# Performance work log

Hardware: AMD Instinct MI355X
Metric: run time of the kernel (lower is better)

Reference implementation:

```python
import jax, jax.numpy as jnp
import numpy as np

EMBED_DIM = 768
NUM_HEADS = 12
HEAD_DIM = EMBED_DIM // NUM_HEADS
B, S = 2, 2048


def setup_inputs() -> dict:
    key = jax.random.key(0)
    ks = jax.random.split(key, 6)
    glorot = jnp.sqrt(6.0 / (EMBED_DIM + EMBED_DIM)).astype(jnp.float32)
    x = jax.random.normal(ks[0], (B, S, EMBED_DIM), dtype=jnp.float32)
    mask = jnp.zeros((1, 1, S, S), dtype=jnp.float32)  # additive mask, 0 = no masking
    Wq = jax.random.uniform(ks[1], (EMBED_DIM, EMBED_DIM), jnp.float32, -glorot, glorot)
    Wk = jax.random.uniform(ks[2], (EMBED_DIM, EMBED_DIM), jnp.float32, -glorot, glorot)
    Wv = jax.random.uniform(ks[3], (EMBED_DIM, EMBED_DIM), jnp.float32, -glorot, glorot)
    Wo = jax.random.uniform(ks[4], (EMBED_DIM, EMBED_DIM), jnp.float32, -glorot, glorot)
    bo = jnp.zeros((EMBED_DIM,), dtype=jnp.float32)
    return {"x": x, "mask": mask, "Wq": Wq, "Wk": Wk, "Wv": Wv, "Wo": Wo, "bo": bo}


def reference(x, mask, Wq, Wk, Wv, Wo, bo):
    b, s, _ = x.shape
    # Q/K/V projections (no bias), split into heads: [b, h, s, d]
    def split_heads(t):
        return t.reshape(b, s, NUM_HEADS, HEAD_DIM).transpose(0, 2, 1, 3)
    q = split_heads(x @ Wq)
    k = split_heads(x @ Wk)
    v = split_heads(x @ Wv)
    scale = 1.0 / jnp.sqrt(jnp.float32(HEAD_DIM))
    logits = jnp.einsum('bhqd,bhkd->bhqk', q, k) * scale  # [b, h, s, s]
    logits = logits + mask * (-1e9)
    weights = jax.nn.softmax(logits, axis=-1)
    attn = jnp.einsum('bhqk,bhkd->bhqd', weights, v)
    concat = attn.transpose(0, 2, 1, 3).reshape(b, s, EMBED_DIM)
    return concat @ Wo + bo
```

## Files before the change

kernel.cpp:

```cpp
#include <hip/hip_runtime.h>


typedef __bf16 bf16_t;
typedef bf16_t bf16x8 __attribute__((ext_vector_type(8)));
typedef bf16_t bf16x4 __attribute__((ext_vector_type(4)));
typedef float f32x4 __attribute__((ext_vector_type(4)));
typedef _Float16 f16x4 __attribute__((ext_vector_type(4)));
typedef _Float16 f16x8 __attribute__((ext_vector_type(8)));
typedef __fp16 hf2 __attribute__((ext_vector_type(2)));

#define SC2 0.1803368801111137f
#define DEFER_THR 44.0f

__device__ __forceinline__ float bf2f(unsigned short u) {
  union { unsigned int i; float f; } x;
  x.i = ((unsigned int)u) << 16;
  return x.f;
}

__device__ __forceinline__ float fexp2(float x) {
  return __builtin_amdgcn_exp2f(x);
}

__device__ __forceinline__ void glds16(const bf16_t* g, bf16_t* l) {
  __builtin_amdgcn_global_load_lds(
      (const __attribute__((address_space(1))) void*)g,
      (__attribute__((address_space(3))) void*)l, 16, 0, 0);
}

__device__ __forceinline__ int detect_bf16_flag(const unsigned short* x) {
  const int lane = threadIdx.x & 63;
  const uint4* p = (const uint4*)x;
  uint4 a = p[lane * 2];
  uint4 b = p[lane * 2 + 1];
  unsigned int w[8] = {a.x, a.y, a.z, a.w, b.x, b.y, b.z, b.w};
  unsigned int big = 0;
#pragma unroll
  for (int i = 0; i < 8; i++) {
    unsigned int e0 = (w[i] >> 7) & 0xFF, e1 = (w[i] >> 23) & 0xFF;
    big |= (e0 > 0x88u) | (e1 > 0x88u);
  }
  unsigned long long bal = __ballot(big != 0u);
  return bal == 0ULL ? 1 : 0;
}

__global__ void k_prep(const void* __restrict__ x, const void* __restrict__ mask,
                       const void* __restrict__ Wq, const void* __restrict__ Wk,
                       const void* __restrict__ Wv, const void* __restrict__ Wo,
                       bf16_t* __restrict__ xb, bf16_t* __restrict__ wqkvT,
                       bf16_t* __restrict__ woT, int* __restrict__ mflags) {
  __shared__ float ts[32][33];
  __shared__ int snz;
  const int blk = blockIdx.x;
  const int f = detect_bf16_flag((const unsigned short*)x);

  if (blk < 1536) {
    if (f) return;
    int i = blk * 256 + threadIdx.x;
    const float* xf = (const float*)x + (size_t)i * 8;
    bf16x8 v;
#pragma unroll
    for (int j = 0; j < 8; j++) v[j] = (bf16_t)xf[j];
    *(bf16x8*)(xb + (size_t)i * 8) = v;
  } else if (blk < 3840) {
    const int t = blk - 1536;
    const int z = t / 576, r = t % 576, kt = r / 24, nt = r % 24;
    const void* wsrc = (z == 0) ? Wq : (z == 1) ? Wk : (z == 2) ? Wv : Wo;
    bf16_t* dst = (z < 3) ? (wqkvT + (size_t)z * 768 * 768) : woT;
    const int c = threadIdx.x & 31, r0 = threadIdx.x >> 5;
#pragma unroll
    for (int i = 0; i < 4; i++) {
      int kr = kt * 32 + r0 + i * 8;
      float v;
      if (f) v = bf2f(((const unsigned short*)wsrc)[(size_t)kr * 768 + nt * 32 + c]);
      else   v = ((const float*)wsrc)[(size_t)kr * 768 + nt * 32 + c];
      ts[r0 + i * 8][c] = v;
    }
    __syncthreads();
#pragma unroll
    for (int i = 0; i < 4; i++) {
      int nr = nt * 32 + r0 + i * 8;
      dst[(size_t)nr * 768 + kt * 32 + c] = (bf16_t)ts[c][r0 + i * 8];
    }
  } else {
    const int t = blk - 3840;
    const int qt = t >> 4, ktm = t & 15;
    if (threadIdx.x == 0) snz = 0;
    __syncthreads();
    unsigned int nz = 0;
    if (f) {
#pragma unroll
      for (int i = 0; i < 8; i++) {
        int uidx = i * 256 + threadIdx.x;
        int row = uidx >> 4, col = uidx & 15;
        const uint4* p = (const uint4*)((const char*)mask +
            ((size_t)(qt * 128 + row) * 2048 + ktm * 128) * 2 + col * 16);
        uint4 v = *p;
        nz |= ((v.x | v.y | v.z | v.w) & 0x7fff7fffu);
      }
    } else {
#pragma unroll
      for (int i = 0; i < 16; i++) {
        int uidx = i * 256 + threadIdx.x;
        int row = uidx >> 5, col = uidx & 31;
        const uint4* p = (const uint4*)((const char*)mask +
            ((size_t)(qt * 128 + row) * 2048 + ktm * 128) * 4 + col * 16);
        uint4 v = *p;
        nz |= ((v.x | v.y | v.z | v.w) & 0x7fffffffu);
      }
    }
    if (nz) snz = 1;
    __syncthreads();
    if (threadIdx.x == 0) mflags[qt * 16 + ktm] = snz;
  }
}

__global__ __launch_bounds__(256, 3) void k_gemmQKV(
    const bf16_t* __restrict__ xb, const bf16_t* __restrict__ Bm,
    bf16_t* __restrict__ Qd, char* __restrict__ Kd, char* __restrict__ Vt,
    const unsigned short* __restrict__ xdet) {
  __shared__ __align__(16) char smem[32768];
  _Float16* Tb = (_Float16*)smem;

  const int f = detect_bf16_flag(xdet);
  const bf16_t* A = f ? (const bf16_t*)xdet : xb;

  const int tid = threadIdx.x;
  const int n0 = blockIdx.x * 128, m0 = blockIdx.y * 128;
  const int r = tid >> 2, c8 = (tid & 3) << 3;
  const bf16_t* Ag = A + (size_t)(m0 + r) * 768 + c8;
  const bf16_t* Bg = Bm + (size_t)(n0 + r) * 768 + c8;
  const int wid = tid >> 6, lane = tid & 63;
  const int wm = (wid >> 1) << 6, wn = (wid & 1) << 6;
  const int lr = lane & 15, quad = lane >> 4, lk = quad << 3, g4 = quad << 2;

  f32x4 acc[4][4];
  const f32x4 z = {0.f, 0.f, 0.f, 0.f};
#pragma unroll
  for (int i = 0; i < 4; i++)
#pragma unroll
    for (int j = 0; j < 4; j++) acc[i][j] = z;

  {
    bf16_t* A0 = (bf16_t*)smem;
    bf16_t* B0 = (bf16_t*)(smem + 16384);
    glds16(Ag, A0 + wid * 512);
    glds16(Ag + (size_t)64 * 768, A0 + 2048 + wid * 512);
    glds16(Bg, B0 + wid * 512);
    glds16(Bg + (size_t)64 * 768, B0 + 2048 + wid * 512);
  }
  __syncthreads();

  for (int s = 0; s < 24; s++) {
    if (s < 23) {
      const int k0 = (s + 1) * 32;
      bf16_t* An = (bf16_t*)(smem + ((s + 1) & 1) * 8192);
      bf16_t* Bn = (bf16_t*)(smem + 16384 + ((s + 1) & 1) * 8192);
      glds16(Ag + k0, An + wid * 512);
      glds16(Ag + (size_t)64 * 768 + k0, An + 2048 + wid * 512);
      glds16(Bg + k0, Bn + wid * 512);
      glds16(Bg + (size_t)64 * 768 + k0, Bn + 2048 + wid * 512);
    }
    const bf16_t* As = (const bf16_t*)(smem + (s & 1) * 8192);
    const bf16_t* Bs = (const bf16_t*)(smem + 16384 + (s & 1) * 8192);
    bf16x8 af[4], bf_[4];
#pragma unroll
    for (int t = 0; t < 4; t++) af[t]  = *(const bf16x8*)&As[(wm + t * 16 + lr) * 32 + lk];
#pragma unroll
    for (int t = 0; t < 4; t++) bf_[t] = *(const bf16x8*)&Bs[(wn + t * 16 + lr) * 32 + lk];
#pragma unroll
    for (int i = 0; i < 4; i++)
#pragma unroll
      for (int j = 0; j < 4; j++)
        acc[i][j] = __builtin_amdgcn_mfma_f32_16x16x32_bf16(af[i], bf_[j], acc[i][j], 0, 0, 0);
    __syncthreads();
  }

  if (n0 < 768) {
    const int bb = m0 >> 11;
#pragma unroll
    for (int i = 0; i < 4; i++)
#pragma unroll
      for (int j = 0; j < 4; j++) {
        const int rc = n0 + wn + j * 16 + lr;
        const int hh = rc >> 6, dd = rc & 63;
        const size_t base = (((size_t)bb * 12 + hh) * 2048) * 64 + dd;
#pragma unroll
        for (int reg = 0; reg < 4; reg++) {
          const int s = (m0 & 2047) + wm + i * 16 + g4 + reg;
          Qd[base + (size_t)s * 64] = (bf16_t)acc[i][j][reg];
        }
      }
  } else if (n0 < 1536) {
    const int nb = n0 - 768;
    const int bb = m0 >> 11;
    const int g = ((m0 & 2047) + wm) >> 6;
#pragma unroll
    for (int i = 0; i < 4; i++) {
#pragma unroll
      for (int j = 0; j < 4; j++) {
        const int rc = nb + wn + j * 16 + lr;
        const int hh = rc >> 6, dd = rc & 63;
        const size_t tbase = ((size_t)((bb * 12 + hh) * 32 + g)) << 13;
        const int doff = ((dd >> 5) << 10) + (((dd >> 3) & 3) << 8) + ((dd & 7) << 1);
#pragma unroll
        for (int reg = 0; reg < 4; reg++) {
          const int sig = ((i >> 1) << 5) + ((quad & 1) << 4) +
                          (((((i & 1) << 1) | (quad >> 1))) << 2) + reg;
          *(bf16_t*)(Kd + tbase + ((sig >> 4) << 11) + ((sig & 15) << 4) + doff) =
              (bf16_t)acc[i][j][reg];
        }
      }
    }
  } else {
    const int bb = m0 >> 11;
#pragma unroll
    for (int half = 0; half < 2; half++) {
      if ((wid & 1) == half) {
#pragma unroll
        for (int j = 0; j < 4; j++) {
          const int d_l = j * 16 + lr;
#pragma unroll
          for (int i = 0; i < 4; i++)
#pragma unroll
            for (int reg = 0; reg < 4; reg++)
              Tb[d_l * 136 + wm + i * 16 + g4 + reg] = (_Float16)acc[i][j][reg];
        }
      }
      __syncthreads();
      const int row = tid >> 2, cc = (tid & 3) * 32;
      const int vcol = (n0 - 1536) + half * 64 + row;
      const int hh = vcol >> 6;
      const int g = ((m0 & 2047) + cc) >> 6;
      const int koff2 = (cc & 63) * 2;
      char* vb = Vt + (((size_t)((bb * 12 + hh) * 32 + g)) << 13) + (row << 7);
#pragma unroll
      for (int u = 0; u < 4; u++)
        *(uint4*)(vb + ((koff2 + u * 16) ^ ((row & 7) << 4))) =
            *(const uint4*)&Tb[row * 136 + cc + u * 8];
      __syncthreads();
    }
  }
}

__global__ __launch_bounds__(256, 4) void k_flash(
    const bf16_t* __restrict__ Qd, const char* __restrict__ Kd,
    const char* __restrict__ Vt, const void* __restrict__ mask,
    const int* __restrict__ mflags, const unsigned short* __restrict__ xdet,
    bf16_t* __restrict__ attn) {
  __shared__ __align__(16) char sm[32768];

  const int tid = threadIdx.x, wid = tid >> 6, lane = tid & 63;
  const int lr = lane & 15, quad = lane >> 4, lk = quad << 3, g4 = quad << 2;

  const int lin = blockIdx.x;
  const int gx = lin & 7, ww = lin >> 3;
  const int hb = gx * 3 + (ww >> 5);
  const int h = hb % 12, bb = hb / 12;
  const int qt = ww & 31;

  const size_t bh = (size_t)bb * 12 + h;
  const char* Kg = Kd + (bh << 18);
  const char* Vg = Vt + (bh << 18);

  const char* kgl = Kg + wid * 2048 + lane * 16;
  const char* vgl = Vg + wid * 2048 + lane * 16;

#define STAGE(t, buf)                                                      \
  {                                                                        \
    const size_t o_ = (size_t)(t) * 8192;                                  \
    glds16((const bf16_t*)(kgl + o_),        (bf16_t*)((buf) + wid * 2048));        \
    glds16((const bf16_t*)(kgl + o_ + 1024), (bf16_t*)((buf) + wid * 2048 + 1024)); \
    glds16((const bf16_t*)(vgl + o_),        (bf16_t*)((buf) + 8192 + wid * 2048)); \
    glds16((const bf16_t*)(vgl + o_ + 1024), (bf16_t*)((buf) + 8192 + wid * 2048 + 1024)); \
  }

  STAGE(0, sm);

  const bf16_t* Qh = Qd + bh * 2048 * 64;
  const int q0 = qt * 64 + wid * 16;
  const int mbf = detect_bf16_flag(xdet);
  const int* mfrow = mflags + (qt >> 1) * 16;
  int mbits = 0;
#pragma unroll
  for (int t = 0; t < 16; t++) mbits |= (mfrow[t] != 0) << t;

  const bf16x8 qf0 = *(const bf16x8*)&Qh[(size_t)(q0 + lr) * 64 + lk];
  const bf16x8 qf1 = *(const bf16x8*)&Qh[(size_t)(q0 + lr) * 64 + 32 + lk];

  f16x8 ones8;
#pragma unroll
  for (int j = 0; j < 8; j++) ones8[j] = (_Float16)1.f;

  const int vxo0 = (quad * 16) ^ ((lr & 7) << 4);
  const int vxo1 = (64 + quad * 16) ^ ((lr & 7) << 4);

  const f32x4 z = {0.f, 0.f, 0.f, 0.f};
  f32x4 ot[4];
#pragma unroll
  for (int dt = 0; dt < 4; dt++) ot[dt] = z;
  float mrow = -1e30f, lrow = 0.f;

  __syncthreads();

  for (int s = 0; s < 32; s++) {
    if (s < 31) STAGE(s + 1, sm + (((s + 1) & 1) << 14));

    const char* Kc = sm + ((s & 1) << 14);
    const char* Vc = Kc + 8192;

    f32x4 sv[4];
#pragma unroll
    for (int ct = 0; ct < 4; ct++) sv[ct] = z;
    __builtin_amdgcn_s_setprio(1);
#pragma unroll
    for (int ct = 0; ct < 4; ct++) {
      bf16x8 kf0 = *(const bf16x8*)(Kc + ct * 2048 + lane * 16);
      bf16x8 kf1 = *(const bf16x8*)(Kc + ct * 2048 + 1024 + lane * 16);
      sv[ct] = __builtin_amdgcn_mfma_f32_16x16x32_bf16(kf0, qf0, sv[ct], 0, 0, 0);
      sv[ct] = __builtin_amdgcn_mfma_f32_16x16x32_bf16(kf1, qf1, sv[ct], 0, 0, 0);
    }
    __builtin_amdgcn_s_setprio(0);

    if ((mbits >> (s >> 1)) & 1) {
#pragma unroll
      for (int ct = 0; ct < 4; ct++)
#pragma unroll
        for (int reg = 0; reg < 4; reg++) {
          const int kk = ((ct >> 1) << 5) + (quad << 3) + ((ct & 1) << 2) + reg;
          size_t mi = (size_t)(q0 + lr) * 2048 + s * 64 + kk;
          float mv = mbf ? bf2f(((const unsigned short*)mask)[mi])
                         : ((const float*)mask)[mi];
          sv[ct][reg] -= 8e9f * mv;
        }
    }

    float t = fmaxf(
        fmaxf(fmaxf(fmaxf(sv[0][0], sv[0][1]), fmaxf(sv[0][2], sv[0][3])),
              fmaxf(fmaxf(sv[1][0], sv[1][1]), fmaxf(sv[1][2], sv[1][3]))),
        fmaxf(fmaxf(fmaxf(sv[2][0], sv[2][1]), fmaxf(sv[2][2], sv[2][3])),
              fmaxf(fmaxf(sv[3][0], sv[3][1]), fmaxf(sv[3][2], sv[3][3]))));
    t = fmaxf(t, __shfl_xor(t, 16));
    t = fmaxf(t, __shfl_xor(t, 32));
    if (__ballot(t > mrow + DEFER_THR)) {
      const float mnew = fmaxf(mrow, t);
      const float alpha = fexp2((mrow - mnew) * SC2);
#pragma unroll
      for (int dt = 0; dt < 4; dt++)
#pragma unroll
        for (int reg = 0; reg < 4; reg++) ot[dt][reg] *= alpha;
      lrow *= alpha;
      mrow = mnew;
    }
    const float mS = mrow * SC2;

    f16x8 pb8[2];
#pragma unroll
    for (int c2 = 0; c2 < 2; c2++) {
      union { hf2 h[4]; f16x8 v; } u;
#pragma unroll
      for (int hh2 = 0; hh2 < 2; hh2++) {
        const int ct = c2 * 2 + hh2;
        float p0 = fexp2(fmaf(sv[ct][0], SC2, -mS));
        float p1 = fexp2(fmaf(sv[ct][1], SC2, -mS));
        float p2 = fexp2(fmaf(sv[ct][2], SC2, -mS));
        float p3 = fexp2(fmaf(sv[ct][3], SC2, -mS));
        u.h[hh2 * 2 + 0] = __builtin_amdgcn_cvt_pkrtz(p0, p1);
        u.h[hh2 * 2 + 1] = __builtin_amdgcn_cvt_pkrtz(p2, p3);
      }
      pb8[c2] = u.v;
    }

    f32x4 asum = z;
    __builtin_amdgcn_s_setprio(1);
#pragma unroll
    for (int c2 = 0; c2 < 2; c2++) {
      const int vxo = c2 ? vxo1 : vxo0;
      asum = __builtin_amdgcn_mfma_f32_16x16x32_f16(ones8, pb8[c2], asum, 0, 0, 0);
#pragma unroll
      for (int dt = 0; dt < 4; dt++) {
        f16x8 va = *(const f16x8*)(Vc + (dt * 16 + lr) * 128 + vxo);
        ot[dt] = __builtin_amdgcn_mfma_f32_16x16x32_f16(va, pb8[c2], ot[dt], 0, 0, 0);
      }
    }
    __builtin_amdgcn_s_setprio(0);
    lrow += asum[0];
    __syncthreads();
  }
#undef STAGE

  const float inv = 1.0f / lrow;
  bf16_t* arow = attn + ((size_t)bb * 2048 + q0 + lr) * 768 + h * 64 + g4;
#pragma unroll
  for (int dt = 0; dt < 4; dt++) {
    bf16x4 v;
#pragma unroll
    for (int reg = 0; reg < 4; reg++) v[reg] = (bf16_t)(ot[dt][reg] * inv);
    *(bf16x4*)(arow + dt * 16) = v;
  }
}

__global__ __launch_bounds__(256, 3) void k_gemm2(
    const bf16_t* __restrict__ A, const bf16_t* __restrict__ Bm,
    const void* __restrict__ bo, const unsigned short* __restrict__ xdet,
    float* __restrict__ outF, unsigned short* __restrict__ outH) {
  __shared__ __align__(16) char smem[32768];

  const int tid = threadIdx.x, wid = tid >> 6, lane = tid & 63;
  const int n0 = blockIdx.x * 64, m0 = blockIdx.y * 64;
  const int wm = (wid >> 1) << 5, wn = (wid & 1) << 5;
  const int lr = lane & 15, lk = (lane >> 4) << 3, g4 = (lane >> 4) << 2;
  const bf16_t* Ag = A + (size_t)(m0 + (tid >> 2)) * 768 + ((tid & 3) << 3);
  const bf16_t* Bg = Bm + (size_t)(n0 + (tid >> 2)) * 768 + ((tid & 3) << 3);

  f32x4 acc[2][2];
  const f32x4 z = {0.f, 0.f, 0.f, 0.f};
#pragma unroll
  for (int i = 0; i < 2; i++)
#pragma unroll
    for (int j = 0; j < 2; j++) acc[i][j] = z;

  {
    bf16_t* A0 = (bf16_t*)smem;
    bf16_t* B0 = (bf16_t*)(smem + 16384);
    glds16(Ag, A0 + wid * 512);
    glds16(Ag + 32, A0 + 2048 + wid * 512);
    glds16(Bg, B0 + wid * 512);
    glds16(Bg + 32, B0 + 2048 + wid * 512);
  }
  __syncthreads();

  for (int s = 0; s < 12; s++) {
    if (s < 11) {
      const int k0 = (s + 1) * 64;
      bf16_t* An = (bf16_t*)(smem + ((s + 1) & 1) * 8192);
      bf16_t* Bn = (bf16_t*)(smem + 16384 + ((s + 1) & 1) * 8192);
      glds16(Ag + k0, An + wid * 512);
      glds16(Ag + k0 + 32, An + 2048 + wid * 512);
      glds16(Bg + k0, Bn + wid * 512);
      glds16(Bg + k0 + 32, Bn + 2048 + wid * 512);
    }
#pragma unroll
    for (int kc = 0; kc < 2; kc++) {
      const bf16_t* As = (const bf16_t*)(smem + (s & 1) * 8192) + kc * 2048;
      const bf16_t* Bs = (const bf16_t*)(smem + 16384 + (s & 1) * 8192) + kc * 2048;
      bf16x8 af[2], bf_[2];
#pragma unroll
      for (int i = 0; i < 2; i++) af[i]  = *(const bf16x8*)&As[(wm + i * 16 + lr) * 32 + lk];
#pragma unroll
      for (int j = 0; j < 2; j++) bf_[j] = *(const bf16x8*)&Bs[(wn + j * 16 + lr) * 32 + lk];
#pragma unroll
      for (int i = 0; i < 2; i++)
#pragma unroll
        for (int j = 0; j < 2; j++)
          acc[i][j] = __builtin_amdgcn_mfma_f32_16x16x32_bf16(af[i], bf_[j], acc[i][j], 0, 0, 0);
    }
    __syncthreads();
  }

  const int obf = detect_bf16_flag(xdet);
#pragma unroll
  for (int i = 0; i < 2; i++)
#pragma unroll
    for (int j = 0; j < 2; j++) {
      const int nn = n0 + wn + j * 16 + lr;
      const float bv = obf ? bf2f(((const unsigned short*)bo)[nn])
                           : ((const float*)bo)[nn];
#pragma unroll
      for (int reg = 0; reg < 4; reg++) {
        const int m = m0 + wm + i * 16 + g4 + reg;
        const float v = acc[i][j][reg] + bv;
        if (obf) outH[(size_t)m * 768 + nn] = __builtin_bit_cast(unsigned short, (bf16_t)v);
        else     outF[(size_t)m * 768 + nn] = v;
      }
    }
}

extern "C" void kernel_launch(void* const* d_in, const int* in_sizes, int n_in,
                              void* d_out, int out_size, void* d_ws, size_t ws_size,
                              hipStream_t stream) {
  (void)in_sizes; (void)n_in; (void)out_size; (void)ws_size;
  const void* x    = d_in[0];
  const void* mask = d_in[1];
  const void* Wq   = d_in[2];
  const void* Wk   = d_in[3];
  const void* Wv   = d_in[4];
  const void* Wo   = d_in[5];
  const void* bo   = d_in[6];

  char* w = (char*)d_ws;
  size_t off = 0;
  auto take = [&](size_t b) -> void* {
    void* p = w + off;
    off = (off + b + 255) & ~(size_t)255;
    return p;
  };
  int*      mflags = (int*)take(256 * 4);
  bf16_t*   wqkvT  = (bf16_t*)take((size_t)2304 * 768 * 2);
  bf16_t*   woT    = (bf16_t*)take((size_t)768 * 768 * 2);
  bf16_t*   xb     = (bf16_t*)take((size_t)4096 * 768 * 2);
  bf16_t*   Qd     = (bf16_t*)take((size_t)3145728 * 2);
  char*     Kd     = (char*)take((size_t)3145728 * 2);
  char*     Vt     = (char*)take((size_t)3145728 * 2);
  bf16_t*   attn   = xb;

  k_prep<<<4096, 256, 0, stream>>>(x, mask, Wq, Wk, Wv, Wo, xb, wqkvT, woT, mflags);
  k_gemmQKV<<<dim3(18, 32), 256, 0, stream>>>(xb, wqkvT, Qd, Kd, Vt,
                                              (const unsigned short*)x);
  k_flash<<<768, 256, 0, stream>>>(Qd, Kd, Vt, mask, mflags,
                                   (const unsigned short*)x, attn);
  k_gemm2<<<dim3(12, 64), 256, 0, stream>>>(attn, woT, bo, (const unsigned short*)x,
                                            (float*)d_out, (unsigned short*)d_out);
}
```

Measured before the change: 172.2 us.

## Software-pipeline QK^T one tile ahead of softmax and PV in flash kernel

Restructures the flash-attention loop so the QK^T MFMAs for tile s+1 are issued while softmax and PV for tile s run, with separate K and V double buffers and K prefetched two tiles ahead. Two score register sets alternate through a 2x manually unrolled loop. This aims to hide the exp/max latency behind matrix-core work. It raises register pressure, so launch bounds drop from 4 to 3 waves per SIMD, which lowers occupancy.

```diff
diff --git a/kernel.cpp b/kernel.cpp
--- a/kernel.cpp
+++ b/kernel.cpp
@@ -243,7 +243,7 @@
   }
 }
 
-__global__ __launch_bounds__(256, 4) void k_flash(
+__global__ __launch_bounds__(256, 3) void k_flash(
     const bf16_t* __restrict__ Qd, const char* __restrict__ Kd,
     const char* __restrict__ Vt, const void* __restrict__ mask,
     const int* __restrict__ mflags, const unsigned short* __restrict__ xdet,
@@ -266,16 +266,24 @@
   const char* kgl = Kg + wid * 2048 + lane * 16;
   const char* vgl = Vg + wid * 2048 + lane * 16;
 
-#define STAGE(t, buf)                                                      \
-  {                                                                        \
-    const size_t o_ = (size_t)(t) * 8192;                                  \
-    glds16((const bf16_t*)(kgl + o_),        (bf16_t*)((buf) + wid * 2048));        \
-    glds16((const bf16_t*)(kgl + o_ + 1024), (bf16_t*)((buf) + wid * 2048 + 1024)); \
-    glds16((const bf16_t*)(vgl + o_),        (bf16_t*)((buf) + 8192 + wid * 2048)); \
-    glds16((const bf16_t*)(vgl + o_ + 1024), (bf16_t*)((buf) + 8192 + wid * 2048 + 1024)); \
-  }
-
-  STAGE(0, sm);
+#define STAGE_K(t, p)                                                       \
+  {                                                                         \
+    const char* g_ = kgl + ((size_t)(t) << 13);                             \
+    bf16_t* l_ = (bf16_t*)(sm + ((p) << 13) + wid * 2048);                  \
+    glds16((const bf16_t*)g_, l_);                                          \
+    glds16((const bf16_t*)(g_ + 1024), l_ + 512);                           \
+  }
+#define STAGE_V(t, p)                                                       \
+  {                                                                         \
+    const char* g_ = vgl + ((size_t)(t) << 13);                             \
+    bf16_t* l_ = (bf16_t*)(sm + 16384 + ((p) << 13) + wid * 2048);          \
+    glds16((const bf16_t*)g_, l_);                                          \
+    glds16((const bf16_t*)(g_ + 1024), l_ + 512);                           \
+  }
+
+  STAGE_K(0, 0);
+  STAGE_V(0, 0);
+  STAGE_K(1, 1);
 
   const bf16_t* Qh = Qd + bh * 2048 * 64;
   const int q0 = qt * 64 + wid * 16;
@@ -303,91 +311,111 @@
 
   __syncthreads();
 
-  for (int s = 0; s < 32; s++) {
-    if (s < 31) STAGE(s + 1, sm + (((s + 1) & 1) << 14));
-
-    const char* Kc = sm + ((s & 1) << 14);
-    const char* Vc = Kc + 8192;
-
-    f32x4 sv[4];
-#pragma unroll
-    for (int ct = 0; ct < 4; ct++) sv[ct] = z;
-    __builtin_amdgcn_s_setprio(1);
+  f32x4 svA[4], svB[4];
+  {
+#pragma unroll
+    for (int ct = 0; ct < 4; ct++) svA[ct] = z;
 #pragma unroll
     for (int ct = 0; ct < 4; ct++) {
-      bf16x8 kf0 = *(const bf16x8*)(Kc + ct * 2048 + lane * 16);
-      bf16x8 kf1 = *(const bf16x8*)(Kc + ct * 2048 + 1024 + lane * 16);
-      sv[ct] = __builtin_amdgcn_mfma_f32_16x16x32_bf16(kf0, qf0, sv[ct], 0, 0, 0);
-      sv[ct] = __builtin_amdgcn_mfma_f32_16x16x32_bf16(kf1, qf1, sv[ct], 0, 0, 0);
-    }
-    __builtin_amdgcn_s_setprio(0);
-
-    if ((mbits >> (s >> 1)) & 1) {
-#pragma unroll
-      for (int ct = 0; ct < 4; ct++)
-#pragma unroll
-        for (int reg = 0; reg < 4; reg++) {
-          const int kk = ((ct >> 1) << 5) + (quad << 3) + ((ct & 1) << 2) + reg;
-          size_t mi = (size_t)(q0 + lr) * 2048 + s * 64 + kk;
-          float mv = mbf ? bf2f(((const unsigned short*)mask)[mi])
-                         : ((const float*)mask)[mi];
-          sv[ct][reg] -= 8e9f * mv;
-        }
-    }
-
-    float t = fmaxf(
-        fmaxf(fmaxf(fmaxf(sv[0][0], sv[0][1]), fmaxf(sv[0][2], sv[0][3])),
-              fmaxf(fmaxf(sv[1][0], sv[1][1]), fmaxf(sv[1][2], sv[1][3]))),
-        fmaxf(fmaxf(fmaxf(sv[2][0], sv[2][1]), fmaxf(sv[2][2], sv[2][3])),
-              fmaxf(fmaxf(sv[3][0], sv[3][1]), fmaxf(sv[3][2], sv[3][3]))));
-    t = fmaxf(t, __shfl_xor(t, 16));
-    t = fmaxf(t, __shfl_xor(t, 32));
-    if (__ballot(t > mrow + DEFER_THR)) {
-      const float mnew = fmaxf(mrow, t);
-      const float alpha = fexp2((mrow - mnew) * SC2);
-#pragma unroll
-      for (int dt = 0; dt < 4; dt++)
-#pragma unroll
-        for (int reg = 0; reg < 4; reg++) ot[dt][reg] *= alpha;
-      lrow *= alpha;
-      mrow = mnew;
-    }
-    const float mS = mrow * SC2;
-
-    f16x8 pb8[2];
-#pragma unroll
-    for (int c2 = 0; c2 < 2; c2++) {
-      union { hf2 h[4]; f16x8 v; } u;
-#pragma unroll
-      for (int hh2 = 0; hh2 < 2; hh2++) {
-        const int ct = c2 * 2 + hh2;
-        float p0 = fexp2(fmaf(sv[ct][0], SC2, -mS));
-        float p1 = fexp2(fmaf(sv[ct][1], SC2, -mS));
-        float p2 = fexp2(fmaf(sv[ct][2], SC2, -mS));
-        float p3 = fexp2(fmaf(sv[ct][3], SC2, -mS));
-        u.h[hh2 * 2 + 0] = __builtin_amdgcn_cvt_pkrtz(p0, p1);
-        u.h[hh2 * 2 + 1] = __builtin_amdgcn_cvt_pkrtz(p2, p3);
-      }
-      pb8[c2] = u.v;
-    }
-
-    f32x4 asum = z;
-    __builtin_amdgcn_s_setprio(1);
-#pragma unroll
-    for (int c2 = 0; c2 < 2; c2++) {
-      const int vxo = c2 ? vxo1 : vxo0;
-      asum = __builtin_amdgcn_mfma_f32_16x16x32_f16(ones8, pb8[c2], asum, 0, 0, 0);
-#pragma unroll
-      for (int dt = 0; dt < 4; dt++) {
-        f16x8 va = *(const f16x8*)(Vc + (dt * 16 + lr) * 128 + vxo);
-        ot[dt] = __builtin_amdgcn_mfma_f32_16x16x32_f16(va, pb8[c2], ot[dt], 0, 0, 0);
-      }
-    }
-    __builtin_amdgcn_s_setprio(0);
-    lrow += asum[0];
-    __syncthreads();
-  }
-#undef STAGE
+      bf16x8 kf0 = *(const bf16x8*)(sm + ct * 2048 + lane * 16);
+      bf16x8 kf1 = *(const bf16x8*)(sm + ct * 2048 + 1024 + lane * 16);
+      svA[ct] = __builtin_amdgcn_mfma_f32_16x16x32_bf16(kf0, qf0, svA[ct], 0, 0, 0);
+      svA[ct] = __builtin_amdgcn_mfma_f32_16x16x32_bf16(kf1, qf1, svA[ct], 0, 0, 0);
+    }
+  }
+  __syncthreads();
+
+#define FLASH_BODY(S, SVC, SVN)                                              \
+  {                                                                          \
+    const int s_ = (S);                                                      \
+    if (s_ + 2 < 32) STAGE_K(s_ + 2, (s_) & 1);                              \
+    if (s_ + 1 < 32) STAGE_V(s_ + 1, (s_ + 1) & 1);                          \
+    if (s_ + 1 < 32) {                                                       \
+      const char* Kn = sm + (((s_ + 1) & 1) << 13);                          \
+      SVN[0] = z; SVN[1] = z; SVN[2] = z; SVN[3] = z;                        \
+      __builtin_amdgcn_s_setprio(1);                                         \
+      _Pragma("unroll")                                                      \
+      for (int ct = 0; ct < 4; ct++) {                                       \
+        bf16x8 kf0 = *(const bf16x8*)(Kn + ct * 2048 + lane * 16);           \
+        bf16x8 kf1 = *(const bf16x8*)(Kn + ct * 2048 + 1024 + lane * 16);    \
+        SVN[ct] = __builtin_amdgcn_mfma_f32_16x16x32_bf16(kf0, qf0, SVN[ct], 0, 0, 0); \
+        SVN[ct] = __builtin_amdgcn_mfma_f32_16x16x32_bf16(kf1, qf1, SVN[ct], 0, 0, 0); \
+      }                                                                      \
+      __builtin_amdgcn_s_setprio(0);                                         \
+    }                                                                        \
+    if ((mbits >> (s_ >> 1)) & 1) {                                          \
+      _Pragma("unroll")                                                      \
+      for (int ct = 0; ct < 4; ct++) {                                       \
+        _Pragma("unroll")                                                    \
+        for (int reg = 0; reg < 4; reg++) {                                  \
+          const int kk = ((ct >> 1) << 5) + (quad << 3) + ((ct & 1) << 2) + reg; \
+          size_t mi = (size_t)(q0 + lr) * 2048 + s_ * 64 + kk;               \
+          float mv = mbf ? bf2f(((const unsigned short*)mask)[mi])           \
+                         : ((const float*)mask)[mi];                         \
+          SVC[ct][reg] -= 8e9f * mv;                                         \
+        }                                                                    \
+      }                                                                      \
+    }                                                                        \
+    float t_ = fmaxf(                                                        \
+        fmaxf(fmaxf(fmaxf(SVC[0][0], SVC[0][1]), fmaxf(SVC[0][2], SVC[0][3])), \
+              fmaxf(fmaxf(SVC[1][0], SVC[1][1]), fmaxf(SVC[1][2], SVC[1][3]))), \
+        fmaxf(fmaxf(fmaxf(SVC[2][0], SVC[2][1]), fmaxf(SVC[2][2], SVC[2][3])), \
+              fmaxf(fmaxf(SVC[3][0], SVC[3][1]), fmaxf(SVC[3][2], SVC[3][3])))); \
+    t_ = fmaxf(t_, __shfl_xor(t_, 16));                                      \
+    t_ = fmaxf(t_, __shfl_xor(t_, 32));                                      \
+    if (__ballot(t_ > mrow + DEFER_THR)) {                                   \
+      const float mnew = fmaxf(mrow, t_);                                    \
+      const float alpha = fexp2((mrow - mnew) * SC2);                        \
+      _Pragma("unroll")                                                      \
+      for (int dt = 0; dt < 4; dt++) {                                       \
+        _Pragma("unroll")                                                    \
+        for (int reg = 0; reg < 4; reg++) ot[dt][reg] *= alpha;              \
+      }                                                                      \
+      lrow *= alpha;                                                         \
+      mrow = mnew;                                                           \
+    }                                                                        \
+    const float mS = mrow * SC2;                                             \
+    f16x8 pb8[2];                                                            \
+    _Pragma("unroll")                                                        \
+    for (int c2 = 0; c2 < 2; c2++) {                                         \
+      union { hf2 hh[4]; f16x8 v; } u;                                       \
+      _Pragma("unroll")                                                      \
+      for (int hh2 = 0; hh2 < 2; hh2++) {                                    \
+        const int ct = c2 * 2 + hh2;                                         \
+        float p0 = fexp2(fmaf(SVC[ct][0], SC2, -mS));                        \
+        float p1 = fexp2(fmaf(SVC[ct][1], SC2, -mS));                        \
+        float p2 = fexp2(fmaf(SVC[ct][2], SC2, -mS));                        \
+        float p3 = fexp2(fmaf(SVC[ct][3], SC2, -mS));                        \
+        u.hh[hh2 * 2 + 0] = __builtin_amdgcn_cvt_pkrtz(p0, p1);              \
+        u.hh[hh2 * 2 + 1] = __builtin_amdgcn_cvt_pkrtz(p2, p3);              \
+      }                                                                      \
+      pb8[c2] = u.v;                                                         \
+    }                                                                        \
+    const char* Vc = sm + 16384 + ((s_ & 1) << 13);                          \
+    f32x4 asum = z;                                                          \
+    __builtin_amdgcn_s_setprio(1);                                           \
+    _Pragma("unroll")                                                        \
+    for (int c2 = 0; c2 < 2; c2++) {                                         \
+      const int vxo = c2 ? vxo1 : vxo0;                                      \
+      asum = __builtin_amdgcn_mfma_f32_16x16x32_f16(ones8, pb8[c2], asum, 0, 0, 0); \
+      _Pragma("unroll")                                                      \
+      for (int dt = 0; dt < 4; dt++) {                                       \
+        f16x8 va = *(const f16x8*)(Vc + (dt * 16 + lr) * 128 + vxo);         \
+        ot[dt] = __builtin_amdgcn_mfma_f32_16x16x32_f16(va, pb8[c2], ot[dt], 0, 0, 0); \
+      }                                                                      \
+    }                                                                        \
+    __builtin_amdgcn_s_setprio(0);                                           \
+    lrow += asum[0];                                                         \
+    if (s_ < 31) __syncthreads();                                            \
+  }
+
+  for (int s2 = 0; s2 < 32; s2 += 2) {
+    FLASH_BODY(s2, svA, svB);
+    FLASH_BODY(s2 + 1, svB, svA);
+  }
+#undef FLASH_BODY
+#undef STAGE_K
+#undef STAGE_V
 
   const float inv = 1.0f / lrow;
   bf16_t* arow = attn + ((size_t)bb * 2048 + q0 + lr) * 768 + h * 64 + g4;
```

Result: no change. 172.9 us (+0.4%).
